# Kernel optimization log

Measured on AMD Instinct MI355X. Metric: run time of the kernel, lower is better.

## Reference

```python
import jax, jax.numpy as jnp
import numpy as np

B, L, HID = 4, 2048, 2048
H, D = 16, 128
BASE = 10000.0
NEG = -1e30


def _rope_tables(seq_len, dim, dtype):
    # inv_freq: (dim/2,), emb = concat(freqs, freqs): (L, dim)
    inv_freq = 1.0 / (BASE ** (jnp.arange(0, dim, 2, dtype=jnp.float32) / dim))
    t = jnp.arange(seq_len, dtype=jnp.float32)
    freqs = t[:, None] * inv_freq[None, :]          # (L, dim/2)
    emb = jnp.concatenate([freqs, freqs], axis=-1)  # (L, dim)
    return jnp.cos(emb).astype(dtype), jnp.sin(emb).astype(dtype)


def _rotate_half(x):
    x1, x2 = x[..., : x.shape[-1] // 2], x[..., x.shape[-1] // 2 :]
    return jnp.concatenate([-x2, x1], axis=-1)


def setup_inputs() -> dict:
    key = jax.random.key(0)
    k1, k2, k3 = jax.random.split(key, 3)
    x = jax.random.normal(k1, (B, L, HID), dtype=jnp.float32)
    # qkv init std = sqrt(2/(5*hidden)); fc xavier std ~ sqrt(2/(in+out))
    Wqkv = jax.random.normal(k2, (HID, 3 * H * D), dtype=jnp.float32) * np.sqrt(2.0 / (5.0 * HID))
    Wo = jax.random.normal(k3, (H * D, HID), dtype=jnp.float32) * np.sqrt(2.0 / (H * D + HID))
    return {"x": x, "Wqkv": Wqkv, "Wo": Wo}


def reference(x, Wqkv, Wo):
    b, l, _ = x.shape
    qkv = (x @ Wqkv).reshape(b, l, 3, H, D).transpose(2, 0, 3, 1, 4)  # (3,b,h,l,d)
    q, k, v = qkv[0], qkv[1], qkv[2]
    cos, sin = _rope_tables(l, D, x.dtype)  # (l, D) each, broadcasts over (b,h,l,d)
    q = q * cos + _rotate_half(q) * sin
    k = k * cos + _rotate_half(k) * sin
    scale = 1.0 / np.sqrt(D)
    scores = jnp.einsum("bhqd,bhkd->bhqk", q, k) * scale  # (b,h,l,l)
    causal = jnp.tril(jnp.ones((l, l), dtype=bool))
    scores = jnp.where(causal, scores, NEG)
    att = jax.nn.softmax(scores, axis=-1)
    out = jnp.einsum("bhqk,bhkd->bhqd", att, v)  # (b,h,l,d)
    out = out.transpose(0, 2, 1, 3).reshape(b, l, H * D)
    return out @ Wo
```

## Files before the change

kernel.cpp:

```cpp
#include <hip/hip_runtime.h>
#include <hip/hip_bf16.h>
#include <stdint.h>

typedef unsigned short ushort_t;
typedef __bf16 bf16x8 __attribute__((ext_vector_type(8)));
typedef float    f32x4 __attribute__((ext_vector_type(4)));
typedef float   f32x16 __attribute__((ext_vector_type(16)));
typedef unsigned short us4 __attribute__((ext_vector_type(4)));
typedef unsigned int ui4 __attribute__((ext_vector_type(4)));

#define QK_SCALE 0.12751744f
#define NEG_BIG  -1e30f

#define BARRIER() do { asm volatile("" ::: "memory"); __builtin_amdgcn_s_barrier(); asm volatile("" ::: "memory"); } while (0)
#define VMCNT(N)  asm volatile("s_waitcnt vmcnt(" #N ")" ::: "memory")
#define MFMA16(d, a, b) d = __builtin_amdgcn_mfma_f32_16x16x32_bf16(a, b, d, 0, 0, 0)

__device__ __forceinline__ unsigned short f2bf(float f) {
    union { float f; unsigned int u; } v; v.f = f;
    unsigned int u = v.u;
    return (unsigned short)((u + 0x7FFFu + ((u >> 16) & 1u)) >> 16);
}

__device__ __forceinline__ unsigned int pk2bf(float a, float b) {
    unsigned int r;
    asm("v_cvt_pk_bf16_f32 %0, %1, %2" : "=v"(r) : "v"(a), "v"(b));
    return r;
}

__device__ __forceinline__ void gload16(const void* g, void* l) {
    __builtin_amdgcn_global_load_lds(
        (__attribute__((address_space(1))) void*)(uintptr_t)g,
        (__attribute__((address_space(3))) void*)(uint32_t)(uintptr_t)l,
        16, 0, 0);
}


__global__ __launch_bounds__(256) void cvt_bf16_kernel(
    const float4* __restrict__ in, us4* __restrict__ out, int n4) {
    int i = blockIdx.x * 256 + threadIdx.x;
    if (i >= n4) return;
    float4 v = in[i];
    us4 o; o[0] = f2bf(v.x); o[1] = f2bf(v.y); o[2] = f2bf(v.z); o[3] = f2bf(v.w);
    out[i] = o;
}

__global__ __launch_bounds__(256) void transpose_bf16(
    const float* __restrict__ in, ushort_t* __restrict__ out, int R, int C) {
    __shared__ float t[64][65];
    int c0 = blockIdx.x * 64, r0 = blockIdx.y * 64;
    int cc = threadIdx.x & 63, rr = threadIdx.x >> 6;
#pragma unroll
    for (int i = 0; i < 16; ++i) {
        int r = i * 4 + rr;
        t[r][cc] = in[(size_t)(r0 + r) * C + c0 + cc];
    }
    __syncthreads();
#pragma unroll
    for (int i = 0; i < 16; ++i) {
        int r = i * 4 + rr;
        out[(size_t)(c0 + r) * R + r0 + cc] = f2bf(t[cc][r]);
    }
}

__global__ __launch_bounds__(256) void transpose_wqkv(
    const float* __restrict__ in , ushort_t* __restrict__ out ) {
    __shared__ float t[64][65];
    int c0 = blockIdx.x * 64, r0 = blockIdx.y * 64;
    int cc = threadIdx.x & 63, rr = threadIdx.x >> 6;
    int n = c0 + cc;
    int which = n >> 11;
    int src = n;
    if (which < 2) {
        int h = (n >> 7) & 15, p = n & 127;
        int po = (p & 15) | (((p >> 5) & 3) << 4) | (((p >> 4) & 1) << 6);
        src = (which << 11) + (h << 7) + po;
    }
#pragma unroll
    for (int i = 0; i < 16; ++i) {
        int r = i * 4 + rr;
        t[r][cc] = in[(size_t)(r0 + r) * 6144 + src];
    }
    __syncthreads();
#pragma unroll
    for (int i = 0; i < 16; ++i) {
        int r = i * 4 + rr;
        out[(size_t)(c0 + r) * 2048 + r0 + cc] = f2bf(t[cc][r]);
    }
}

__global__ __launch_bounds__(256) void rope_table_kernel(float2* __restrict__ rope) {
    int i = blockIdx.x * 256 + threadIdx.x;
    int l = i >> 6, j = i & 63;
    float inv = exp2f((float)j * -0.20762050593046f);
    float f = (float)l * inv;
    rope[i] = make_float2(cosf(f), sinf(f));
}


template <int EPI>
__global__ __launch_bounds__(512, 2)
void gemm256(const ushort_t* __restrict__ A, const ushort_t* __restrict__ Bt,
             int M, int N, int K,
             float* __restrict__ C,
             ushort_t* __restrict__ Qb, ushort_t* __restrict__ Kb,
             ushort_t* __restrict__ Vt, const float2* __restrict__ rope) {
    __shared__ __attribute__((aligned(16))) char lds[131072];

    const int tid  = threadIdx.x;
    const int lane = tid & 63, wid = tid >> 6;
    const int lr = lane & 15, lg = lane >> 4;
    const int wr = wid >> 2, wc = wid & 3;

    const int nbn = N >> 8;
    const int nwg = gridDim.x;
    const int bid = blockIdx.x;
    const int wg  = (bid & 7) * (nwg >> 3) + (bid >> 3);
    const int bm  = wg / nbn, bn = wg % nbn;

    const int srow = tid >> 3;
    const int scol = ((tid & 7) << 4) ^ ((srow & 7) << 4);
    const size_t rowK2 = (size_t)K * 2;
    const char* sA0 = (const char*)A + ((size_t)(bm * 256 + srow)) * rowK2 + scol;
    const char* sA1 = sA0 + 128 * rowK2;
    const char* sB0 = (const char*)Bt + ((size_t)(bn * 256 + srow)) * rowK2 + scol;
    const char* sB1 = sB0 + 128 * rowK2;

    auto stg = [&](const char* s, int ch, int kt, int dst) {
        gload16(s + (size_t)(ch * 64) * rowK2 + (size_t)kt * 128, lds + dst + wid * 1024);
    };

    const int xk0 = (lg * 16) ^ ((lr & 7) << 4);
    const int xk1 = (64 + lg * 16) ^ ((lr & 7) << 4);
    const int rowA = wr * 16384 + lr * 128;
    const int rowB = 32768 + (wc >> 1) * 16384 + ((wc & 1) * 64 + lr) * 128;

    auto rdA = [&](int bu, int mi, int kk) -> bf16x8 {
        return *(const bf16x8*)(lds + bu * 65536 + rowA + mi * 2048 + (kk ? xk1 : xk0));
    };
    auto rdB = [&](int bu, int ni, int kk) -> bf16x8 {
        return *(const bf16x8*)(lds + bu * 65536 + rowB + ni * 2048 + (kk ? xk1 : xk0));
    };

    f32x4 acc[8][4];
#pragma unroll
    for (int m = 0; m < 8; ++m)
#pragma unroll
        for (int n = 0; n < 4; ++n) acc[m][n] = (f32x4){0.f, 0.f, 0.f, 0.f};

    bf16x8 aF[4][2], bF[2][2];

#define RD_A(BU, MH) do { _Pragma("unroll") for (int mi = 0; mi < 4; ++mi) { \
        aF[mi][0] = rdA(BU, (MH)*4 + mi, 0); aF[mi][1] = rdA(BU, (MH)*4 + mi, 1); } } while (0)
#define RD_B(BU, NH) do { _Pragma("unroll") for (int ni = 0; ni < 2; ++ni) { \
        bF[ni][0] = rdB(BU, (NH)*2 + ni, 0); bF[ni][1] = rdB(BU, (NH)*2 + ni, 1); } } while (0)
#define QUAD(MH, NH) do { __builtin_amdgcn_s_setprio(1); \
        _Pragma("unroll") for (int kk = 0; kk < 2; ++kk) \
        _Pragma("unroll") for (int mi = 0; mi < 4; ++mi) \
        _Pragma("unroll") for (int ni = 0; ni < 2; ++ni) \
            MFMA16(acc[(MH)*4 + mi][(NH)*2 + ni], aF[mi][kk], bF[ni][kk]); \
        __builtin_amdgcn_s_setprio(0); } while (0)

    stg(sA0, 0, 0, 0);     stg(sA0, 1, 0, 8192);
    stg(sA1, 0, 0, 16384); stg(sA1, 1, 0, 24576);
    stg(sB0, 0, 0, 32768); stg(sB0, 1, 0, 40960);
    stg(sB1, 0, 0, 49152); stg(sB1, 1, 0, 57344);
    stg(sA0, 1, 1, 73728); stg(sA1, 1, 1, 90112);
    stg(sB0, 0, 1, 98304); stg(sB0, 1, 1, 106496);
    VMCNT(4);
    BARRIER();

    const int NIT = K / 128;
    for (int i = 0; i < NIT; ++i) {
        const int to = 2 * i + 1, te2 = 2 * i + 2, to2 = 2 * i + 3;
        const bool g = (i + 1 < NIT);

        RD_A(0, 0); RD_B(0, 0);
        stg(sB1, 0, to, 114688); stg(sB1, 1, to, 122880);
        BARRIER(); QUAD(0, 0); BARRIER();

        RD_A(0, 1);
        stg(sA0, 0, to, 65536); stg(sA1, 0, to, 81920);
        BARRIER(); QUAD(1, 0); BARRIER();

        RD_B(0, 1);
        if (g) { stg(sA0, 1, te2, 8192); stg(sA1, 1, te2, 24576); }
        BARRIER(); QUAD(1, 1); BARRIER();

        RD_A(0, 0);
        if (g) { stg(sB0, 0, te2, 32768); stg(sB0, 1, te2, 40960); VMCNT(4); }
        else   { VMCNT(0); }
        BARRIER(); QUAD(0, 1); BARRIER();

        RD_A(1, 0); RD_B(1, 0);
        if (g) { stg(sB1, 0, te2, 49152); stg(sB1, 1, te2, 57344); }
        BARRIER(); QUAD(0, 0); BARRIER();

        RD_A(1, 1);
        if (g) { stg(sA0, 0, te2, 0); stg(sA1, 0, te2, 16384); }
        BARRIER(); QUAD(1, 0); BARRIER();

        RD_B(1, 1);
        if (g) { stg(sA0, 1, to2, 73728); stg(sA1, 1, to2, 90112); }
        BARRIER(); QUAD(1, 1); BARRIER();

        RD_A(1, 0);
        if (g) { stg(sB0, 0, to2, 98304); stg(sB0, 1, to2, 106496); VMCNT(4); }
        BARRIER(); QUAD(0, 1); BARRIER();
    }

#undef RD_A
#undef RD_B
#undef QUAD

    if constexpr (EPI == 0) {
#pragma unroll
        for (int m = 0; m < 8; ++m) {
            int gr0 = bm * 256 + wr * 128 + m * 16 + lg * 4;
#pragma unroll
            for (int n = 0; n < 4; ++n) {
                int gc = bn * 256 + wc * 64 + n * 16 + lr;
#pragma unroll
                for (int r = 0; r < 4; ++r)
                    C[(size_t)(gr0 + r) * N + gc] = acc[m][n][r];
            }
        }
    } else {
        const int hc = bn * 2 + (wc >> 1);
        const int which = hc >> 4, h = hc & 15;
#pragma unroll
        for (int m = 0; m < 8; ++m) {
            int gr0 = bm * 256 + wr * 128 + m * 16 + lg * 4;
            int b = gr0 >> 11, l0 = gr0 & 2047;
            if (which == 2) {
#pragma unroll
                for (int n = 0; n < 4; ++n) {
                    int d = (wc & 1) * 64 + n * 16 + lr;
                    us4 pk;
#pragma unroll
                    for (int r = 0; r < 4; ++r) pk[r] = f2bf(acc[m][n][r]);
                    *(us4*)(Vt + ((size_t)(b * 16 + h) * 128 + d) * 2048 + l0) = pk;
                }
            } else {
                ushort_t* dst = (which == 0) ? Qb : Kb;
                const float sc = (which == 0) ? QK_SCALE : 1.0f;
#pragma unroll
                for (int np = 0; np < 4; np += 2) {
                    int tbl = ((wc & 1) * 2 + (np >> 1)) * 16 + lr;
                    int p1 = (wc & 1) * 64 + np * 16 + lr;
#pragma unroll
                    for (int r = 0; r < 4; ++r) {
                        float2 cs = rope[(size_t)(l0 + r) * 64 + tbl];
                        float x1 = acc[m][np][r], x2 = acc[m][np + 1][r];
                        size_t base = ((size_t)(b * 16 + h) * 2048 + (l0 + r)) * 128;
                        dst[base + p1]      = f2bf((x1 * cs.x - x2 * cs.y) * sc);
                        dst[base + p1 + 16] = f2bf((x2 * cs.x + x1 * cs.y) * sc);
                    }
                }
            }
        }
    }
}


__global__ __attribute__((amdgpu_flat_work_group_size(512, 512), amdgpu_waves_per_eu(2, 2)))
void attn_fwd(const ushort_t* __restrict__ Qb, const ushort_t* __restrict__ Kb,
              const ushort_t* __restrict__ Vt, ushort_t* __restrict__ AO) {
    constexpr int L = 2048;
    __shared__ __attribute__((aligned(16))) char smem[131072];

    const int tid  = threadIdx.x;
    const int lane = tid & 63, wid = tid >> 6;
    const int q_l  = lane & 31;
    const int hi   = lane >> 5;

    const int bid  = blockIdx.x;
    const int hl   = (bid >> 3) & 7;
    const int pr   = bid >> 6;
    const int head = (bid & 7) * 8 + hl;

    const ushort_t* Qh = Qb + (size_t)head * L * 128;
    const char*     KhB = (const char*)(Kb + (size_t)head * L * 128);
    const char*     VhB = (const char*)(Vt + (size_t)head * 128 * L);
    const int b = head >> 4, h = head & 15;

    int rKV[4], cK[4], cV[4];
#pragma unroll
    for (int i = 0; i < 4; ++i) {
        rKV[i] = wid * 16 + i * 4 + (lane >> 4);
        cK[i]  = ((lane & 15) << 4) ^ ((rKV[i] & 7) << 4);
        cV[i]  = cK[i];
    }
    const int kdst = wid * 4096;
    const int vdst = 32768 + wid * 4096;

    for (int ph = 0; ph < 2; ++ph) {
        const int s    = ph ? (7 - pr) : pr;
        const int q0w  = s * 256 + wid * 32;
        const int nch  = 2 * s + 2;

        bf16x8 qf[8];
#pragma unroll
        for (int sb = 0; sb < 8; ++sb)
            qf[sb] = *(const bf16x8*)(Qh + (size_t)(q0w + q_l) * 128 + sb * 16 + hi * 8);

        f32x16 o[4];
#pragma unroll
        for (int d0 = 0; d0 < 4; ++d0) o[d0] = (f32x16)(0.f);
        float m_ = -__builtin_inff(), l_ = 0.f;

        __syncthreads();
#pragma unroll
        for (int i = 0; i < 4; ++i) {
            gload16(KhB + (size_t)rKV[i] * 256 + cK[i], smem + kdst + i * 1024);
            gload16(VhB + (size_t)rKV[i] * 4096 + cV[i], smem + vdst + i * 1024);
        }

        for (int c = 0; c < nch; ++c) {
            __syncthreads();
            const int kb = (c & 1) * 65536;
            const int nb = ((c + 1) & 1) * 65536;
            if (c + 1 < nch) {
                const int kn = 128 * (c + 1);
#pragma unroll
                for (int i = 0; i < 4; ++i) {
                    gload16(KhB + (size_t)(kn + rKV[i]) * 256 + cK[i], smem + nb + kdst + i * 1024);
                    gload16(VhB + (size_t)rKV[i] * 4096 + (size_t)kn * 2 + cV[i], smem + nb + vdst + i * 1024);
                }
            }

#pragma unroll
            for (int sub = 0; sub < 2; ++sub) {
                const int k0 = 128 * c + 64 * sub;
                if (k0 > q0w + 31) continue;
                const bool do1 = (k0 + 32 <= q0w + 31);
                const int kloc = sub * 64;

                f32x16 s0, s1;
                {
                    bf16x8 kf[8];
#pragma unroll
                    for (int sb = 0; sb < 8; ++sb) {
                        int off = kb + (kloc + q_l) * 256 + ((sb * 32 + hi * 16) ^ ((q_l & 7) << 4));
                        kf[sb] = *(const bf16x8*)(smem + off);
                    }
                    f32x16 sA = (f32x16)(0.f), sB = (f32x16)(0.f);
#pragma unroll
                    for (int sb = 0; sb < 8; sb += 2) {
                        sA = __builtin_amdgcn_mfma_f32_32x32x16_bf16(kf[sb],     qf[sb],     sA, 0, 0, 0);
                        sB = __builtin_amdgcn_mfma_f32_32x32x16_bf16(kf[sb + 1], qf[sb + 1], sB, 0, 0, 0);
                    }
                    s0 = sA + sB;
                }
                if (do1) {
                    bf16x8 kf[8];
#pragma unroll
                    for (int sb = 0; sb < 8; ++sb) {
                        int off = kb + (kloc + 32 + q_l) * 256 + ((sb * 32 + hi * 16) ^ ((q_l & 7) << 4));
                        kf[sb] = *(const bf16x8*)(smem + off);
                    }
                    f32x16 sA = (f32x16)(0.f), sB = (f32x16)(0.f);
#pragma unroll
                    for (int sb = 0; sb < 8; sb += 2) {
                        sA = __builtin_amdgcn_mfma_f32_32x32x16_bf16(kf[sb],     qf[sb],     sA, 0, 0, 0);
                        sB = __builtin_amdgcn_mfma_f32_32x32x16_bf16(kf[sb + 1], qf[sb + 1], sB, 0, 0, 0);
                    }
                    s1 = sA + sB;
                }

                if (k0 + 31 > q0w) {
#pragma unroll
                    for (int r = 0; r < 16; ++r) {
                        int crow = (r & 3) + 8 * (r >> 2) + 4 * hi;
                        if (k0 + crow > q0w + q_l) s0[r] = NEG_BIG;
                    }
                }
                if (do1 && (k0 + 63 > q0w)) {
#pragma unroll
                    for (int r = 0; r < 16; ++r) {
                        int crow = (r & 3) + 8 * (r >> 2) + 4 * hi;
                        if (k0 + 32 + crow > q0w + q_l) s1[r] = NEG_BIG;
                    }
                }

                float t8[8];
#pragma unroll
                for (int r = 0; r < 8; ++r) t8[r] = fmaxf(s0[r], s0[r + 8]);
                if (do1)
#pragma unroll
                    for (int r = 0; r < 8; ++r) t8[r] = fmaxf(t8[r], fmaxf(s1[r], s1[r + 8]));
#pragma unroll
                for (int r = 0; r < 4; ++r) t8[r] = fmaxf(t8[r], t8[r + 4]);
                float tmax = fmaxf(fmaxf(t8[0], t8[1]), fmaxf(t8[2], t8[3]));
                tmax = fmaxf(tmax, __shfl_xor(tmax, 32, 64));

                if (!__all(tmax <= m_ + 8.f)) {
                    float mn = fmaxf(m_, tmax);
                    float alpha = exp2f(m_ - mn);
                    m_ = mn;
                    l_ *= alpha;
#pragma unroll
                    for (int d0 = 0; d0 < 4; ++d0)
#pragma unroll
                        for (int r = 0; r < 16; ++r) o[d0][r] *= alpha;
                }

                float rs = 0.f;
#pragma unroll
                for (int r = 0; r < 16; ++r) { s0[r] = exp2f(s0[r] - m_); rs += s0[r]; }
                if (do1)
#pragma unroll
                    for (int r = 0; r < 16; ++r) { s1[r] = exp2f(s1[r] - m_); rs += s1[r]; }
                rs += __shfl_xor(rs, 32, 64);
                l_ += rs;

                bf16x8 pfA[2], pfB[2];
                {
                    unsigned int pk[8], po[8];
#pragma unroll
                    for (int i = 0; i < 8; ++i) pk[i] = pk2bf(s0[2 * i], s0[2 * i + 1]);
#pragma unroll
                    for (int i = 0; i < 8; ++i) po[i] = __shfl_xor(pk[i], 32, 64);
#pragma unroll
                    for (int ks = 0; ks < 2; ++ks) {
                        ui4 dw;
                        dw[0] = hi ? po[ks * 4 + 2] : pk[ks * 4 + 0];
                        dw[1] = hi ? po[ks * 4 + 3] : pk[ks * 4 + 1];
                        dw[2] = hi ? pk[ks * 4 + 2] : po[ks * 4 + 0];
                        dw[3] = hi ? pk[ks * 4 + 3] : po[ks * 4 + 1];
                        pfA[ks] = __builtin_bit_cast(bf16x8, dw);
                    }
                }
                if (do1) {
                    unsigned int pk[8], po[8];
#pragma unroll
                    for (int i = 0; i < 8; ++i) pk[i] = pk2bf(s1[2 * i], s1[2 * i + 1]);
#pragma unroll
                    for (int i = 0; i < 8; ++i) po[i] = __shfl_xor(pk[i], 32, 64);
#pragma unroll
                    for (int ks = 0; ks < 2; ++ks) {
                        ui4 dw;
                        dw[0] = hi ? po[ks * 4 + 2] : pk[ks * 4 + 0];
                        dw[1] = hi ? po[ks * 4 + 3] : pk[ks * 4 + 1];
                        dw[2] = hi ? pk[ks * 4 + 2] : po[ks * 4 + 0];
                        dw[3] = hi ? pk[ks * 4 + 3] : po[ks * 4 + 1];
                        pfB[ks] = __builtin_bit_cast(bf16x8, dw);
                    }
                }

                const int vb = kb + 32768;
#pragma unroll
                for (int d0 = 0; d0 < 4; ++d0) {
                    int d = d0 * 32 + q_l;
#pragma unroll
                    for (int ks = 0; ks < 2; ++ks) {
                        int off = vb + d * 256 + ((sub * 128 + ks * 32 + hi * 16) ^ ((d & 7) << 4));
                        bf16x8 vf = *(const bf16x8*)(smem + off);
                        o[d0] = __builtin_amdgcn_mfma_f32_32x32x16_bf16(vf, pfA[ks], o[d0], 0, 0, 0);
                    }
                    if (do1) {
#pragma unroll
                        for (int ks = 0; ks < 2; ++ks) {
                            int off = vb + d * 256 + ((sub * 128 + (2 + ks) * 32 + hi * 16) ^ ((d & 7) << 4));
                            bf16x8 vf = *(const bf16x8*)(smem + off);
                            o[d0] = __builtin_amdgcn_mfma_f32_32x32x16_bf16(vf, pfB[ks], o[d0], 0, 0, 0);
                        }
                    }
                }
            }
        }

        const float inv = 1.f / l_;
        const size_t rowbase = ((size_t)(b * 2048 + q0w + q_l)) * 2048 + h * 128;
#pragma unroll
        for (int d0 = 0; d0 < 4; ++d0)
#pragma unroll
            for (int g = 0; g < 4; ++g) {
                us4 v;
#pragma unroll
                for (int r = 0; r < 4; ++r) v[r] = f2bf(o[d0][g * 4 + r] * inv);
                *(us4*)(AO + rowbase + d0 * 32 + g * 8 + hi * 4) = v;
            }
    }
}


extern "C" void kernel_launch(void* const* d_in, const int* in_sizes, int n_in,
                              void* d_out, int out_size, void* d_ws, size_t ws_size,
                              hipStream_t stream) {
    const float* x    = (const float*)d_in[0];
    const float* Wqkv = (const float*)d_in[1];
    const float* Wo   = (const float*)d_in[2];
    float* out = (float*)d_out;

    char* w = (char*)d_ws;
    ushort_t* xb   = (ushort_t*)(w);
    ushort_t* W1t  = (ushort_t*)(w + 33554432);
    ushort_t* Wot  = (ushort_t*)(w + 58720256);
    ushort_t* Qb   = (ushort_t*)(w + 67108864);
    ushort_t* Kbf  = (ushort_t*)(w + 100663296);
    ushort_t* Vt   = (ushort_t*)(w + 134217728);
    ushort_t* AO   = (ushort_t*)(w + 167772160);
    float2*   rope = (float2*)(w + 201326592);

    cvt_bf16_kernel<<<16384, 256, 0, stream>>>((const float4*)x, (us4*)xb, 4194304);
    transpose_wqkv<<<dim3(96, 32), 256, 0, stream>>>(Wqkv, W1t);
    transpose_bf16<<<dim3(32, 32), 256, 0, stream>>>(Wo, Wot, 2048, 2048);
    rope_table_kernel<<<512, 256, 0, stream>>>(rope);

    gemm256<1><<<768, 512, 0, stream>>>(xb, W1t, 8192, 6144, 2048,
                                        nullptr, Qb, Kbf, Vt, rope);
    attn_fwd<<<256, 512, 0, stream>>>(Qb, Kbf, Vt, AO);
    gemm256<0><<<256, 512, 0, stream>>>(AO, Wot, 8192, 2048, 2048,
                                        out, nullptr, nullptr, nullptr, nullptr);
}
```

Baseline: 420.3 us.

## Drop pre-compute barriers in GEMM loop and use permlane32 swap for P fragments

Removes the barrier before each MFMA quad in the GEMM main loop, leaving one barrier per phase instead of two. The barrier's job is to order LDS reads against the global-to-LDS stages and make staged data visible. In the attention kernel, the shfl_xor-plus-select exchange of packed bf16 probabilities between the two 32-lane halves is replaced with v_permlane32_swap_b32 inline asm. This avoids the ds_bpermute traffic and the per-lane selects, but removing barriers risks LDS read/write races if the remaining synchronisation is not enough.

```diff
diff --git a/kernel.cpp b/kernel.cpp
--- a/kernel.cpp
+++ b/kernel.cpp
@@ -177,36 +177,36 @@
 
         RD_A(0, 0); RD_B(0, 0);
         stg(sB1, 0, to, 114688); stg(sB1, 1, to, 122880);
-        BARRIER(); QUAD(0, 0); BARRIER();
+        QUAD(0, 0); BARRIER();
 
         RD_A(0, 1);
         stg(sA0, 0, to, 65536); stg(sA1, 0, to, 81920);
-        BARRIER(); QUAD(1, 0); BARRIER();
+        QUAD(1, 0); BARRIER();
 
         RD_B(0, 1);
         if (g) { stg(sA0, 1, te2, 8192); stg(sA1, 1, te2, 24576); }
-        BARRIER(); QUAD(1, 1); BARRIER();
+        QUAD(1, 1); BARRIER();
 
         RD_A(0, 0);
         if (g) { stg(sB0, 0, te2, 32768); stg(sB0, 1, te2, 40960); VMCNT(4); }
         else   { VMCNT(0); }
-        BARRIER(); QUAD(0, 1); BARRIER();
+        QUAD(0, 1); BARRIER();
 
         RD_A(1, 0); RD_B(1, 0);
         if (g) { stg(sB1, 0, te2, 49152); stg(sB1, 1, te2, 57344); }
-        BARRIER(); QUAD(0, 0); BARRIER();
+        QUAD(0, 0); BARRIER();
 
         RD_A(1, 1);
         if (g) { stg(sA0, 0, te2, 0); stg(sA1, 0, te2, 16384); }
-        BARRIER(); QUAD(1, 0); BARRIER();
+        QUAD(1, 0); BARRIER();
 
         RD_B(1, 1);
         if (g) { stg(sA0, 1, to2, 73728); stg(sA1, 1, to2, 90112); }
-        BARRIER(); QUAD(1, 1); BARRIER();
+        QUAD(1, 1); BARRIER();
 
         RD_A(1, 0);
         if (g) { stg(sB0, 0, to2, 98304); stg(sB0, 1, to2, 106496); VMCNT(4); }
-        BARRIER(); QUAD(0, 1); BARRIER();
+        QUAD(0, 1); BARRIER();
     }
 
 #undef RD_A
@@ -416,34 +416,30 @@
 
                 bf16x8 pfA[2], pfB[2];
                 {
-                    unsigned int pk[8], po[8];
+                    unsigned int pk[8];
 #pragma unroll
                     for (int i = 0; i < 8; ++i) pk[i] = pk2bf(s0[2 * i], s0[2 * i + 1]);
 #pragma unroll
-                    for (int i = 0; i < 8; ++i) po[i] = __shfl_xor(pk[i], 32, 64);
-#pragma unroll
                     for (int ks = 0; ks < 2; ++ks) {
-                        ui4 dw;
-                        dw[0] = hi ? po[ks * 4 + 2] : pk[ks * 4 + 0];
-                        dw[1] = hi ? po[ks * 4 + 3] : pk[ks * 4 + 1];
-                        dw[2] = hi ? pk[ks * 4 + 2] : po[ks * 4 + 0];
-                        dw[3] = hi ? pk[ks * 4 + 3] : po[ks * 4 + 1];
+                        unsigned int a0 = pk[ks * 4 + 0], b0 = pk[ks * 4 + 2];
+                        unsigned int a1 = pk[ks * 4 + 1], b1 = pk[ks * 4 + 3];
+                        asm("v_permlane32_swap_b32 %0, %1" : "+v"(a0), "+v"(b0));
+                        asm("v_permlane32_swap_b32 %0, %1" : "+v"(a1), "+v"(b1));
+                        ui4 dw; dw[0] = a0; dw[1] = a1; dw[2] = b0; dw[3] = b1;
                         pfA[ks] = __builtin_bit_cast(bf16x8, dw);
                     }
                 }
                 if (do1) {
-                    unsigned int pk[8], po[8];
+                    unsigned int pk[8];
 #pragma unroll
                     for (int i = 0; i < 8; ++i) pk[i] = pk2bf(s1[2 * i], s1[2 * i + 1]);
 #pragma unroll
-                    for (int i = 0; i < 8; ++i) po[i] = __shfl_xor(pk[i], 32, 64);
-#pragma unroll
                     for (int ks = 0; ks < 2; ++ks) {
-                        ui4 dw;
-                        dw[0] = hi ? po[ks * 4 + 2] : pk[ks * 4 + 0];
-                        dw[1] = hi ? po[ks * 4 + 3] : pk[ks * 4 + 1];
-                        dw[2] = hi ? pk[ks * 4 + 2] : po[ks * 4 + 0];
-                        dw[3] = hi ? pk[ks * 4 + 3] : po[ks * 4 + 1];
+                        unsigned int a0 = pk[ks * 4 + 0], b0 = pk[ks * 4 + 2];
+                        unsigned int a1 = pk[ks * 4 + 1], b1 = pk[ks * 4 + 3];
+                        asm("v_permlane32_swap_b32 %0, %1" : "+v"(a0), "+v"(b0));
+                        asm("v_permlane32_swap_b32 %0, %1" : "+v"(a1), "+v"(b1));
+                        ui4 dw; dw[0] = a0; dw[1] = a1; dw[2] = b0; dw[3] = b1;
                         pfB[ks] = __builtin_bit_cast(bf16x8, dw);
                     }
                 }
```

After: 409.5 us (median of 3 runs). 2.6% less time.
